# Performance work log

Measured on AMD Instinct MI355X. Metric: run time of the kernel, lower is better.

## Reference

```python
import jax, jax.numpy as jnp
import numpy as np

N = 100000   # nodes
E = 1600000  # edges (before self-loops)
H1, C1 = 8, 16   # conv1: heads=8, out_channels=16
H2, C2 = 1, 1    # conv2: heads=1, out_channels=1
NEG_SLOPE = 0.2
EPS = 1e-16


def setup_inputs() -> dict:
    key = jax.random.key(0)
    ks = jax.random.split(key, 10)
    s = 0.3
    return {
        "x": jax.random.normal(ks[0], (N, 1), jnp.float32),
        "edge_index": jax.random.randint(ks[1], (2, E), 0, N, dtype=jnp.int64),
        "W1": jax.random.normal(ks[2], (1, H1 * C1), jnp.float32) * s,
        "att_src1": jax.random.normal(ks[3], (1, H1, C1), jnp.float32) * s,
        "att_dst1": jax.random.normal(ks[4], (1, H1, C1), jnp.float32) * s,
        "b1": jax.random.normal(ks[5], (H1 * C1,), jnp.float32) * s,
        "W2": jax.random.normal(ks[6], (H1 * C1, H2 * C2), jnp.float32) * s,
        "att_src2": jax.random.normal(ks[7], (1, H2, C2), jnp.float32) * s,
        "att_dst2": jax.random.normal(ks[8], (1, H2, C2), jnp.float32) * s,
        "b2": jax.random.normal(ks[9], (C2,), jnp.float32) * s,
    }


def gat_conv(x, src, dst, W, att_src, att_dst, bias, heads, ch, concat):
    # Linear projection, split into heads: [N, H, C]
    h = (x @ W).reshape(-1, heads, ch)
    # Per-node attention logits: [N, H]
    a_src = (h * att_src).sum(-1)
    a_dst = (h * att_dst).sum(-1)
    # Edge-wise score with LeakyReLU: [E, H]
    e = jax.nn.leaky_relu(a_src[src] + a_dst[dst], NEG_SLOPE)
    # Segment softmax over incoming edges of each dst node
    m = jax.ops.segment_max(e, dst, num_segments=N)
    ex = jnp.exp(e - m[dst])
    denom = jax.ops.segment_sum(ex, dst, num_segments=N)
    alpha = ex / (denom[dst] + EPS)                      # [E, H]
    # Weighted scatter-add aggregation: [N, H, C]
    out = jax.ops.segment_sum(h[src] * alpha[:, :, None], dst, num_segments=N)
    out = out.reshape(-1, heads * ch) if concat else out.mean(axis=1)
    return out + bias


def reference(x, edge_index, W1, att_src1, att_dst1, b1, W2, att_src2, att_dst2, b2):
    # PyG GATConv default add_self_loops=True
    loop = jnp.arange(N, dtype=edge_index.dtype)
    src = jnp.concatenate([edge_index[0], loop])
    dst = jnp.concatenate([edge_index[1], loop])
    # dropout p=0.6 is identity in eval mode
    h = gat_conv(x, src, dst, W1, att_src1, att_dst1, b1, H1, C1, concat=True)
    h = jax.nn.elu(h)
    out = gat_conv(h, src, dst, W2, att_src2, att_dst2, b2, H2, C2, concat=False)
    return out  # [N, 1]
```

## Files before the change

kernel.cpp:

```cpp
#include <hip/hip_runtime.h>

#define NEG_SLOPE 0.2f
#define EPSV 1e-16f
#define NHEADS 8
#define NCH 16
#define BKT_SHIFT 7
#define BKT_NODES 128
#define CAP 4096
#define BIN_EPB 4096
#define MAX_BKT 800

__global__ __launch_bounds__(256) void gat_bin_kernel(
        const int* __restrict__ ei, int E, int nbuckets,
        int* __restrict__ bkt_cnt, unsigned int* __restrict__ binned) {
    __shared__ int hist[MAX_BKT];
    __shared__ int gbase[MAX_BKT];
    int t = threadIdx.x;
    for (int i = t; i < nbuckets; i += 256) hist[i] = 0;
    __syncthreads();
    int base = blockIdx.x * BIN_EPB;
    int lr[BIN_EPB / 256];
#pragma unroll
    for (int k = 0; k < BIN_EPB / 1024; ++k) {
        int idx = base + k * 1024 + t * 4;
        if (idx + 3 < E) {
            int4 d4 = *(const int4*)(ei + E + idx);
            lr[4 * k + 0] = atomicAdd(&hist[d4.x >> BKT_SHIFT], 1);
            lr[4 * k + 1] = atomicAdd(&hist[d4.y >> BKT_SHIFT], 1);
            lr[4 * k + 2] = atomicAdd(&hist[d4.z >> BKT_SHIFT], 1);
            lr[4 * k + 3] = atomicAdd(&hist[d4.w >> BKT_SHIFT], 1);
        } else {
            for (int u = 0; u < 4; ++u)
                if (idx + u < E)
                    lr[4 * k + u] = atomicAdd(&hist[ei[E + idx + u] >> BKT_SHIFT], 1);
        }
    }
    __syncthreads();
    for (int i = t; i < nbuckets; i += 256) {
        int c = hist[i];
        gbase[i] = c ? (i * CAP + atomicAdd(&bkt_cnt[i], c)) : 0;
    }
    __syncthreads();
#pragma unroll
    for (int k = 0; k < BIN_EPB / 1024; ++k) {
        int idx = base + k * 1024 + t * 4;
        if (idx + 3 < E) {
            int4 s4 = *(const int4*)(ei + idx);
            int4 d4 = *(const int4*)(ei + E + idx);
            binned[gbase[d4.x >> BKT_SHIFT] + lr[4 * k + 0]] =
                ((unsigned int)s4.x << BKT_SHIFT) | (unsigned int)(d4.x & (BKT_NODES - 1));
            binned[gbase[d4.y >> BKT_SHIFT] + lr[4 * k + 1]] =
                ((unsigned int)s4.y << BKT_SHIFT) | (unsigned int)(d4.y & (BKT_NODES - 1));
            binned[gbase[d4.z >> BKT_SHIFT] + lr[4 * k + 2]] =
                ((unsigned int)s4.z << BKT_SHIFT) | (unsigned int)(d4.z & (BKT_NODES - 1));
            binned[gbase[d4.w >> BKT_SHIFT] + lr[4 * k + 3]] =
                ((unsigned int)s4.w << BKT_SHIFT) | (unsigned int)(d4.w & (BKT_NODES - 1));
        } else {
            for (int u = 0; u < 4; ++u)
                if (idx + u < E) {
                    unsigned int s = (unsigned int)ei[idx + u];
                    int d = ei[E + idx + u];
                    binned[gbase[d >> BKT_SHIFT] + lr[4 * k + u]] =
                        (s << BKT_SHIFT) | (unsigned int)(d & (BKT_NODES - 1));
                }
        }
    }
}

__global__ __launch_bounds__(256) void gat_gather1_kernel(
        int N, const float* __restrict__ x,
        unsigned int* __restrict__ binned, const int* __restrict__ bkt_cnt,
        const float* __restrict__ W1, const float* __restrict__ as1,
        const float* __restrict__ ad1, const float* __restrict__ b1,
        const float* __restrict__ W2, float* __restrict__ h2out,
        int* __restrict__ row_start, int* __restrict__ row_deg) {
    __shared__ unsigned int ed[CAP];
    __shared__ int cnt[BKT_NODES], offs[BKT_NODES], cur[BKT_NODES];
    __shared__ float xloc[BKT_NODES];
    __shared__ float sS1[NHEADS], sD1[NHEADS];
    int b = blockIdx.x, t = threadIdx.x;
    if (t < NHEADS) {
        float s = 0.f, d = 0.f;
        for (int c = 0; c < NCH; ++c) {
            float w = W1[t * NCH + c];
            s += w * as1[t * NCH + c];
            d += w * ad1[t * NCH + c];
        }
        sS1[t] = s; sD1[t] = d;
    }
    if (t < BKT_NODES) {
        int node = (b << BKT_SHIFT) + t;
        xloc[t] = (node < N) ? x[node] : 0.f;
        cnt[t] = 0;
    }
    __syncthreads();
    int nE = bkt_cnt[b]; if (nE > CAP) nE = CAP;
    const unsigned int* bb = binned + (size_t)b * CAP;
    for (int j0 = 0; j0 < nE; j0 += 1024) {
        int idx = j0 + t * 4;
        if (idx + 3 < nE) {
            uint4 qv = *(const uint4*)(bb + idx);
            atomicAdd(&cnt[qv.x & (BKT_NODES - 1)], 1);
            atomicAdd(&cnt[qv.y & (BKT_NODES - 1)], 1);
            atomicAdd(&cnt[qv.z & (BKT_NODES - 1)], 1);
            atomicAdd(&cnt[qv.w & (BKT_NODES - 1)], 1);
        } else {
            for (int u = 0; u < 4; ++u)
                if (idx + u < nE) atomicAdd(&cnt[bb[idx + u] & (BKT_NODES - 1)], 1);
        }
    }
    __syncthreads();
    if (t < BKT_NODES) offs[t] = cnt[t];
    __syncthreads();
    for (int o = 1; o < BKT_NODES; o <<= 1) {
        int v = (t < BKT_NODES && t >= o) ? offs[t - o] : 0;
        __syncthreads();
        if (t < BKT_NODES) offs[t] += v;
        __syncthreads();
    }
    if (t < BKT_NODES) cur[t] = offs[t] - cnt[t];
    __syncthreads();
    for (int j0 = 0; j0 < nE; j0 += 1024) {
        int idx = j0 + t * 4;
        if (idx + 3 < nE) {
            uint4 qv = *(const uint4*)(bb + idx);
            ed[atomicAdd(&cur[qv.x & (BKT_NODES - 1)], 1)] = qv.x >> BKT_SHIFT;
            ed[atomicAdd(&cur[qv.y & (BKT_NODES - 1)], 1)] = qv.y >> BKT_SHIFT;
            ed[atomicAdd(&cur[qv.z & (BKT_NODES - 1)], 1)] = qv.z >> BKT_SHIFT;
            ed[atomicAdd(&cur[qv.w & (BKT_NODES - 1)], 1)] = qv.w >> BKT_SHIFT;
        } else {
            for (int u = 0; u < 4; ++u)
                if (idx + u < nE) {
                    unsigned int v = bb[idx + u];
                    ed[atomicAdd(&cur[v & (BKT_NODES - 1)], 1)] = v >> BKT_SHIFT;
                }
        }
    }
    __syncthreads();
    for (int j0 = 0; j0 < nE; j0 += 1024) {
        int idx = j0 + t * 4;
        if (idx + 3 < nE) {
            *(uint4*)(binned + (size_t)b * CAP + idx) = *(const uint4*)(ed + idx);
        } else {
            for (int u = 0; u < 4; ++u)
                if (idx + u < nE) binned[(size_t)b * CAP + idx + u] = ed[idx + u];
        }
    }
    int loc = t >> 1;
    int q = t & 1;
    int deg = cnt[loc];
    int ob = offs[loc] - deg;
    int lo = ob + ((deg * q) >> 1);
    int hi = ob + ((deg * (q + 1)) >> 1);
    float xd = xloc[loc];
    float S1[NHEADS], A[NHEADS], den[NHEADS], num[NHEADS];
#pragma unroll
    for (int h = 0; h < NHEADS; ++h) {
        S1[h] = sS1[h];
        A[h] = xd * sD1[h];
        den[h] = 0.f;
        num[h] = 0.f;
    }
    int j = lo;
    for (; j + 2 <= hi; j += 2) {
        unsigned int e0 = ed[j], e1 = ed[j + 1];
        float x0 = x[e0], x1 = x[e1];
#pragma unroll
        for (int h = 0; h < NHEADS; ++h) {
            float ea = x0 * S1[h] + A[h]; ea = ea > 0.f ? ea : NEG_SLOPE * ea;
            float eb = x1 * S1[h] + A[h]; eb = eb > 0.f ? eb : NEG_SLOPE * eb;
            float fa = __expf(ea), fb = __expf(eb);
            den[h] += fa + fb;
            num[h] += fa * x0 + fb * x1;
        }
    }
    if (j < hi) {
        unsigned int e0 = ed[j];
        float x0 = x[e0];
#pragma unroll
        for (int h = 0; h < NHEADS; ++h) {
            float ea = x0 * S1[h] + A[h];
            ea = ea > 0.f ? ea : NEG_SLOPE * ea;
            float fa = __expf(ea);
            den[h] += fa;
            num[h] += fa * x0;
        }
    }
#pragma unroll
    for (int h = 0; h < NHEADS; ++h) {
        den[h] += __shfl_xor(den[h], 1);
        num[h] += __shfl_xor(num[h], 1);
    }
    if (q == 0) {
        int node = (b << BKT_SHIFT) + loc;
        if (node < N) {
            row_start[node] = b * CAP + ob;
            row_deg[node] = deg;
            float xn = xd;
            float acc = 0.f;
#pragma unroll
            for (int h = 0; h < NHEADS; ++h) {
                float e = xn * (S1[h] + sD1[h]);
                e = e > 0.f ? e : NEG_SLOPE * e;
                float ex = __expf(e);
                float dsum = den[h] + ex + EPSV;
                float nsum = num[h] + ex * xn;
                float z = nsum / dsum;
#pragma unroll
                for (int c = 0; c < NCH; ++c) {
                    int k = h * NCH + c;
                    float vv = W1[k] * z + b1[k];
                    vv = vv > 0.f ? vv : (__expf(vv) - 1.f);
                    acc += vv * W2[k];
                }
            }
            h2out[node] = acc;
        }
    }
}

__global__ __launch_bounds__(256) void gat_gather2_kernel(
        int N, const float* __restrict__ h2,
        const unsigned int* __restrict__ binned,
        const int* __restrict__ row_start, const int* __restrict__ row_deg,
        const float* __restrict__ as2p, const float* __restrict__ ad2p,
        const float* __restrict__ b2, float* __restrict__ out) {
    int g = blockIdx.x * blockDim.x + threadIdx.x;
    int n = g >> 1;
    int q = g & 1;
    bool valid = (n < N);
    int nc = valid ? n : 0;
    float a_s = as2p[0], a_d = ad2p[0];
    float hn = h2[nc];
    float adc = hn * a_d;
    int st = row_start[nc];
    int dg = valid ? row_deg[nc] : 0;
    int lo = st + ((dg * q) >> 1);
    int hi = st + ((dg * (q + 1)) >> 1);
    float den = 0.f, num = 0.f;
    int j = lo;
    for (; j + 2 <= hi; j += 2) {
        unsigned int e0 = binned[j], e1 = binned[j + 1];
        float h0 = h2[e0], h1 = h2[e1];
        float ea = h0 * a_s + adc; ea = ea > 0.f ? ea : NEG_SLOPE * ea;
        float eb = h1 * a_s + adc; eb = eb > 0.f ? eb : NEG_SLOPE * eb;
        float fa = __expf(ea), fb = __expf(eb);
        den += fa + fb;
        num += fa * h0 + fb * h1;
    }
    if (j < hi) {
        unsigned int e0 = binned[j];
        float h0 = h2[e0];
        float ea = h0 * a_s + adc;
        ea = ea > 0.f ? ea : NEG_SLOPE * ea;
        float fa = __expf(ea);
        den += fa;
        num += fa * h0;
    }
    den += __shfl_xor(den, 1);
    num += __shfl_xor(num, 1);
    if (q == 0 && valid) {
        float e = hn * (a_s + a_d);
        e = e > 0.f ? e : NEG_SLOPE * e;
        float ex = __expf(e);
        out[n] = (num + ex * hn) / (den + ex + EPSV) + b2[0];
    }
}

extern "C" void kernel_launch(void* const* d_in, const int* in_sizes, int n_in,
                              void* d_out, int out_size, void* d_ws, size_t ws_size,
                              hipStream_t stream) {
    const float* x   = (const float*)d_in[0];
    const int*   ei  = (const int*)d_in[1];
    const float* W1  = (const float*)d_in[2];
    const float* as1 = (const float*)d_in[3];
    const float* ad1 = (const float*)d_in[4];
    const float* b1  = (const float*)d_in[5];
    const float* W2  = (const float*)d_in[6];
    const float* as2 = (const float*)d_in[7];
    const float* ad2 = (const float*)d_in[8];
    const float* b2  = (const float*)d_in[9];
    float* out = (float*)d_out;

    int N = in_sizes[0];
    int E = in_sizes[1] / 2;

    int nbuckets = (N + BKT_NODES - 1) >> BKT_SHIFT;
    int nbin     = (E + BIN_EPB - 1) / BIN_EPB;
    int nb2      = (2 * N + 255) / 256;

    float* h2        = (float*)d_ws;
    int*   row_start = (int*)(h2 + N);
    int*   row_deg   = row_start + N;
    int*   bkt_cnt   = row_deg + N;
    size_t ofs = ((size_t)3 * N + nbuckets + 3) & ~(size_t)3;
    unsigned int* binned = (unsigned int*)d_ws + ofs;

    hipMemsetAsync(bkt_cnt, 0, (size_t)nbuckets * sizeof(int), stream);

    gat_bin_kernel<<<nbin, 256, 0, stream>>>(ei, E, nbuckets, bkt_cnt, binned);
    gat_gather1_kernel<<<nbuckets, 256, 0, stream>>>(N, x, binned, bkt_cnt,
                                                     W1, as1, ad1, b1, W2,
                                                     h2, row_start, row_deg);
    gat_gather2_kernel<<<nb2, 256, 0, stream>>>(N, h2, binned, row_start, row_deg,
                                                as2, ad2, b2, out);
}
```

Before: 141.2 us.

## Shard bucket counters, drop CSR writeback, and make layer-2 gather bucket-local

The binning kernel now spreads its global atomic counters over four shards per bucket, each with its own 1024-entry sub-region, to reduce contention on the per-bucket counters. The first gather kernel no longer writes the sorted edge list back to global memory or emits row_start/row_deg, and it replaces the multi-barrier shared-memory scan with a wavefront shuffle scan. The second layer's gather now processes each bucket's unsorted edges directly with shared-memory float atomics into per-node accumulators. This trades the global writeback for LDS atomic contention, and caps each shard at 1024 edges, which could drop edges if a shard overflows.

```diff
diff --git a/kernel.cpp b/kernel.cpp
--- a/kernel.cpp
+++ b/kernel.cpp
@@ -7,6 +7,8 @@
 #define BKT_SHIFT 7
 #define BKT_NODES 128
 #define CAP 4096
+#define QCAP 1024
+#define NSHARD 4
 #define BIN_EPB 4096
 #define MAX_BKT 800
 
@@ -16,6 +18,7 @@
     __shared__ int hist[MAX_BKT];
     __shared__ int gbase[MAX_BKT];
     int t = threadIdx.x;
+    int s = blockIdx.x & (NSHARD - 1);
     for (int i = t; i < nbuckets; i += 256) hist[i] = 0;
     __syncthreads();
     int base = blockIdx.x * BIN_EPB;
@@ -38,7 +41,8 @@
     __syncthreads();
     for (int i = t; i < nbuckets; i += 256) {
         int c = hist[i];
-        gbase[i] = c ? (i * CAP + atomicAdd(&bkt_cnt[i], c)) : 0;
+        gbase[i] = c ? (i * CAP + s * QCAP + atomicAdd(&bkt_cnt[i * NSHARD + s], c))
+                     : 0;
     }
     __syncthreads();
 #pragma unroll
@@ -58,10 +62,10 @@
         } else {
             for (int u = 0; u < 4; ++u)
                 if (idx + u < E) {
-                    unsigned int s = (unsigned int)ei[idx + u];
+                    unsigned int sv = (unsigned int)ei[idx + u];
                     int d = ei[E + idx + u];
                     binned[gbase[d >> BKT_SHIFT] + lr[4 * k + u]] =
-                        (s << BKT_SHIFT) | (unsigned int)(d & (BKT_NODES - 1));
+                        (sv << BKT_SHIFT) | (unsigned int)(d & (BKT_NODES - 1));
                 }
         }
     }
@@ -69,15 +73,15 @@
 
 __global__ __launch_bounds__(256) void gat_gather1_kernel(
         int N, const float* __restrict__ x,
-        unsigned int* __restrict__ binned, const int* __restrict__ bkt_cnt,
+        const unsigned int* __restrict__ binned, const int* __restrict__ bkt_cnt,
         const float* __restrict__ W1, const float* __restrict__ as1,
         const float* __restrict__ ad1, const float* __restrict__ b1,
-        const float* __restrict__ W2, float* __restrict__ h2out,
-        int* __restrict__ row_start, int* __restrict__ row_deg) {
+        const float* __restrict__ W2, float* __restrict__ h2out) {
     __shared__ unsigned int ed[CAP];
     __shared__ int cnt[BKT_NODES], offs[BKT_NODES], cur[BKT_NODES];
     __shared__ float xloc[BKT_NODES];
     __shared__ float sS1[NHEADS], sD1[NHEADS];
+    __shared__ int wtot;
     int b = blockIdx.x, t = threadIdx.x;
     if (t < NHEADS) {
         float s = 0.f, d = 0.f;
@@ -94,62 +98,73 @@
         cnt[t] = 0;
     }
     __syncthreads();
-    int nE = bkt_cnt[b]; if (nE > CAP) nE = CAP;
-    const unsigned int* bb = binned + (size_t)b * CAP;
-    for (int j0 = 0; j0 < nE; j0 += 1024) {
-        int idx = j0 + t * 4;
-        if (idx + 3 < nE) {
-            uint4 qv = *(const uint4*)(bb + idx);
-            atomicAdd(&cnt[qv.x & (BKT_NODES - 1)], 1);
-            atomicAdd(&cnt[qv.y & (BKT_NODES - 1)], 1);
-            atomicAdd(&cnt[qv.z & (BKT_NODES - 1)], 1);
-            atomicAdd(&cnt[qv.w & (BKT_NODES - 1)], 1);
-        } else {
-            for (int u = 0; u < 4; ++u)
-                if (idx + u < nE) atomicAdd(&cnt[bb[idx + u] & (BKT_NODES - 1)], 1);
-        }
-    }
-    __syncthreads();
-    if (t < BKT_NODES) offs[t] = cnt[t];
-    __syncthreads();
-    for (int o = 1; o < BKT_NODES; o <<= 1) {
-        int v = (t < BKT_NODES && t >= o) ? offs[t - o] : 0;
+    int nq[NSHARD];
+#pragma unroll
+    for (int s = 0; s < NSHARD; ++s) {
+        int v = bkt_cnt[b * NSHARD + s];
+        nq[s] = v > QCAP ? QCAP : v;
+    }
+#pragma unroll
+    for (int s = 0; s < NSHARD; ++s) {
+        const unsigned int* bq = binned + (size_t)b * CAP + s * QCAP;
+        int nE = nq[s];
+        for (int idx = t * 4; idx < nE; idx += 1024) {
+            if (idx + 3 < nE) {
+                uint4 qv = *(const uint4*)(bq + idx);
+                atomicAdd(&cnt[qv.x & (BKT_NODES - 1)], 1);
+                atomicAdd(&cnt[qv.y & (BKT_NODES - 1)], 1);
+                atomicAdd(&cnt[qv.z & (BKT_NODES - 1)], 1);
+                atomicAdd(&cnt[qv.w & (BKT_NODES - 1)], 1);
+            } else {
+                for (int u = 0; u < 4; ++u)
+                    if (idx + u < nE) atomicAdd(&cnt[bq[idx + u] & (BKT_NODES - 1)], 1);
+            }
+        }
+    }
+    __syncthreads();
+    {
+        int c = (t < BKT_NODES) ? cnt[t] : 0;
+        int lane = t & 63;
+        int v = c;
+#pragma unroll
+        for (int o = 1; o < 64; o <<= 1) {
+            int u = __shfl_up(v, o);
+            if (lane >= o) v += u;
+        }
+        if (t == 63) wtot = v;
         __syncthreads();
-        if (t < BKT_NODES) offs[t] += v;
-        __syncthreads();
-    }
-    if (t < BKT_NODES) cur[t] = offs[t] - cnt[t];
-    __syncthreads();
-    for (int j0 = 0; j0 < nE; j0 += 1024) {
-        int idx = j0 + t * 4;
-        if (idx + 3 < nE) {
-            uint4 qv = *(const uint4*)(bb + idx);
-            ed[atomicAdd(&cur[qv.x & (BKT_NODES - 1)], 1)] = qv.x >> BKT_SHIFT;
-            ed[atomicAdd(&cur[qv.y & (BKT_NODES - 1)], 1)] = qv.y >> BKT_SHIFT;
-            ed[atomicAdd(&cur[qv.z & (BKT_NODES - 1)], 1)] = qv.z >> BKT_SHIFT;
-            ed[atomicAdd(&cur[qv.w & (BKT_NODES - 1)], 1)] = qv.w >> BKT_SHIFT;
-        } else {
-            for (int u = 0; u < 4; ++u)
-                if (idx + u < nE) {
-                    unsigned int v = bb[idx + u];
-                    ed[atomicAdd(&cur[v & (BKT_NODES - 1)], 1)] = v >> BKT_SHIFT;
-                }
-        }
-    }
-    __syncthreads();
-    for (int j0 = 0; j0 < nE; j0 += 1024) {
-        int idx = j0 + t * 4;
-        if (idx + 3 < nE) {
-            *(uint4*)(binned + (size_t)b * CAP + idx) = *(const uint4*)(ed + idx);
-        } else {
-            for (int u = 0; u < 4; ++u)
-                if (idx + u < nE) binned[(size_t)b * CAP + idx + u] = ed[idx + u];
-        }
-    }
+        if (t < BKT_NODES) {
+            int incl = v + ((t >= 64) ? wtot : 0);
+            offs[t] = incl - c;
+            cur[t] = incl - c;
+        }
+    }
+    __syncthreads();
+#pragma unroll
+    for (int s = 0; s < NSHARD; ++s) {
+        const unsigned int* bq = binned + (size_t)b * CAP + s * QCAP;
+        int nE = nq[s];
+        for (int idx = t * 4; idx < nE; idx += 1024) {
+            if (idx + 3 < nE) {
+                uint4 qv = *(const uint4*)(bq + idx);
+                ed[atomicAdd(&cur[qv.x & (BKT_NODES - 1)], 1)] = qv.x >> BKT_SHIFT;
+                ed[atomicAdd(&cur[qv.y & (BKT_NODES - 1)], 1)] = qv.y >> BKT_SHIFT;
+                ed[atomicAdd(&cur[qv.z & (BKT_NODES - 1)], 1)] = qv.z >> BKT_SHIFT;
+                ed[atomicAdd(&cur[qv.w & (BKT_NODES - 1)], 1)] = qv.w >> BKT_SHIFT;
+            } else {
+                for (int u = 0; u < 4; ++u)
+                    if (idx + u < nE) {
+                        unsigned int v = bq[idx + u];
+                        ed[atomicAdd(&cur[v & (BKT_NODES - 1)], 1)] = v >> BKT_SHIFT;
+                    }
+            }
+        }
+    }
+    __syncthreads();
     int loc = t >> 1;
     int q = t & 1;
     int deg = cnt[loc];
-    int ob = offs[loc] - deg;
+    int ob = offs[loc];
     int lo = ob + ((deg * q) >> 1);
     int hi = ob + ((deg * (q + 1)) >> 1);
     float xd = xloc[loc];
@@ -194,8 +209,6 @@
     if (q == 0) {
         int node = (b << BKT_SHIFT) + loc;
         if (node < N) {
-            row_start[node] = b * CAP + ob;
-            row_deg[node] = deg;
             float xn = xd;
             float acc = 0.f;
 #pragma unroll
@@ -221,49 +234,55 @@
 
 __global__ __launch_bounds__(256) void gat_gather2_kernel(
         int N, const float* __restrict__ h2,
-        const unsigned int* __restrict__ binned,
-        const int* __restrict__ row_start, const int* __restrict__ row_deg,
+        const unsigned int* __restrict__ binned, const int* __restrict__ bkt_cnt,
         const float* __restrict__ as2p, const float* __restrict__ ad2p,
         const float* __restrict__ b2, float* __restrict__ out) {
-    int g = blockIdx.x * blockDim.x + threadIdx.x;
-    int n = g >> 1;
-    int q = g & 1;
-    bool valid = (n < N);
-    int nc = valid ? n : 0;
+    __shared__ float den2[BKT_NODES], num2[BKT_NODES], hloc[BKT_NODES];
+    int b = blockIdx.x, t = threadIdx.x;
+    if (t < BKT_NODES) {
+        int node = (b << BKT_SHIFT) + t;
+        hloc[t] = (node < N) ? h2[node] : 0.f;
+        den2[t] = 0.f;
+        num2[t] = 0.f;
+    }
     float a_s = as2p[0], a_d = ad2p[0];
-    float hn = h2[nc];
-    float adc = hn * a_d;
-    int st = row_start[nc];
-    int dg = valid ? row_deg[nc] : 0;
-    int lo = st + ((dg * q) >> 1);
-    int hi = st + ((dg * (q + 1)) >> 1);
-    float den = 0.f, num = 0.f;
-    int j = lo;
-    for (; j + 2 <= hi; j += 2) {
-        unsigned int e0 = binned[j], e1 = binned[j + 1];
-        float h0 = h2[e0], h1 = h2[e1];
-        float ea = h0 * a_s + adc; ea = ea > 0.f ? ea : NEG_SLOPE * ea;
-        float eb = h1 * a_s + adc; eb = eb > 0.f ? eb : NEG_SLOPE * eb;
-        float fa = __expf(ea), fb = __expf(eb);
-        den += fa + fb;
-        num += fa * h0 + fb * h1;
-    }
-    if (j < hi) {
-        unsigned int e0 = binned[j];
-        float h0 = h2[e0];
-        float ea = h0 * a_s + adc;
-        ea = ea > 0.f ? ea : NEG_SLOPE * ea;
-        float fa = __expf(ea);
-        den += fa;
-        num += fa * h0;
-    }
-    den += __shfl_xor(den, 1);
-    num += __shfl_xor(num, 1);
-    if (q == 0 && valid) {
-        float e = hn * (a_s + a_d);
-        e = e > 0.f ? e : NEG_SLOPE * e;
-        float ex = __expf(e);
-        out[n] = (num + ex * hn) / (den + ex + EPSV) + b2[0];
+    __syncthreads();
+#pragma unroll
+    for (int s = 0; s < NSHARD; ++s) {
+        int nE = bkt_cnt[b * NSHARD + s];
+        if (nE > QCAP) nE = QCAP;
+        const unsigned int* bq = binned + (size_t)b * CAP + s * QCAP;
+        for (int idx = t * 4; idx < nE; idx += 1024) {
+            unsigned int v[4];
+            int nv = 0;
+            if (idx + 3 < nE) {
+                uint4 qv = *(const uint4*)(bq + idx);
+                v[0] = qv.x; v[1] = qv.y; v[2] = qv.z; v[3] = qv.w; nv = 4;
+            } else {
+                for (int u = 0; u < 4; ++u)
+                    if (idx + u < nE) v[nv++] = bq[idx + u];
+            }
+            for (int u = 0; u < nv; ++u) {
+                int loc = v[u] & (BKT_NODES - 1);
+                float hs = h2[v[u] >> BKT_SHIFT];
+                float e = hs * a_s + hloc[loc] * a_d;
+                e = e > 0.f ? e : NEG_SLOPE * e;
+                float ex = __expf(e);
+                atomicAdd(&den2[loc], ex);
+                atomicAdd(&num2[loc], ex * hs);
+            }
+        }
+    }
+    __syncthreads();
+    if (t < BKT_NODES) {
+        int node = (b << BKT_SHIFT) + t;
+        if (node < N) {
+            float hn = hloc[t];
+            float e = hn * (a_s + a_d);
+            e = e > 0.f ? e : NEG_SLOPE * e;
+            float ex = __expf(e);
+            out[node] = (num2[t] + ex * hn) / (den2[t] + ex + EPSV) + b2[0];
+        }
     }
 }
 
@@ -287,21 +306,17 @@
 
     int nbuckets = (N + BKT_NODES - 1) >> BKT_SHIFT;
     int nbin     = (E + BIN_EPB - 1) / BIN_EPB;
-    int nb2      = (2 * N + 255) / 256;
-
-    float* h2        = (float*)d_ws;
-    int*   row_start = (int*)(h2 + N);
-    int*   row_deg   = row_start + N;
-    int*   bkt_cnt   = row_deg + N;
-    size_t ofs = ((size_t)3 * N + nbuckets + 3) & ~(size_t)3;
+
+    float* h2      = (float*)d_ws;
+    int*   bkt_cnt = (int*)(h2 + N);
+    size_t ofs = ((size_t)N + (size_t)NSHARD * nbuckets + 3) & ~(size_t)3;
     unsigned int* binned = (unsigned int*)d_ws + ofs;
 
-    hipMemsetAsync(bkt_cnt, 0, (size_t)nbuckets * sizeof(int), stream);
+    hipMemsetAsync(bkt_cnt, 0, (size_t)NSHARD * nbuckets * sizeof(int), stream);
 
     gat_bin_kernel<<<nbin, 256, 0, stream>>>(ei, E, nbuckets, bkt_cnt, binned);
     gat_gather1_kernel<<<nbuckets, 256, 0, stream>>>(N, x, binned, bkt_cnt,
-                                                     W1, as1, ad1, b1, W2,
-                                                     h2, row_start, row_deg);
-    gat_gather2_kernel<<<nb2, 256, 0, stream>>>(N, h2, binned, row_start, row_deg,
-                                                as2, ad2, b2, out);
+                                                     W1, as1, ad1, b1, W2, h2);
+    gat_gather2_kernel<<<nbuckets, 256, 0, stream>>>(N, h2, binned, bkt_cnt,
+                                                     as2, ad2, b2, out);
 }
```

Result: slower. 153.8 us (+9.0%).

## Shard per-bucket global counters across eight sub-queues and use wave-shuffle scan

Applied to the files above, without the earlier changes.

The binning kernel now spreads each bucket's global atomic counter across eight shards chosen by block index, and each shard writes into its own 512-slot sub-region of the bucket. The aim is to cut contention on the global atomics when many blocks append to the same bucket. The gather kernel reads the eight shard counts and skips the unused gaps between sub-regions. It also replaces the shared-memory Hillis-Steele prefix scan with a wavefront shuffle scan to remove barriers. The cost is a per-shard capacity of 512 edges, which can overflow if the edge distribution is skewed, and some wasted reads over partially filled sub-regions.

```diff
diff --git a/kernel.cpp b/kernel.cpp
--- a/kernel.cpp
+++ b/kernel.cpp
@@ -6,6 +6,9 @@
 #define NCH 16
 #define BKT_SHIFT 7
 #define BKT_NODES 128
+#define NSHARD 8
+#define QSHIFT 9
+#define QCAP 512
 #define CAP 4096
 #define BIN_EPB 4096
 #define MAX_BKT 800
@@ -16,6 +19,7 @@
     __shared__ int hist[MAX_BKT];
     __shared__ int gbase[MAX_BKT];
     int t = threadIdx.x;
+    int s = blockIdx.x & (NSHARD - 1);
     for (int i = t; i < nbuckets; i += 256) hist[i] = 0;
     __syncthreads();
     int base = blockIdx.x * BIN_EPB;
@@ -38,7 +42,8 @@
     __syncthreads();
     for (int i = t; i < nbuckets; i += 256) {
         int c = hist[i];
-        gbase[i] = c ? (i * CAP + atomicAdd(&bkt_cnt[i], c)) : 0;
+        gbase[i] = c ? (i * CAP + s * QCAP + atomicAdd(&bkt_cnt[i * NSHARD + s], c))
+                     : 0;
     }
     __syncthreads();
 #pragma unroll
@@ -58,10 +63,10 @@
         } else {
             for (int u = 0; u < 4; ++u)
                 if (idx + u < E) {
-                    unsigned int s = (unsigned int)ei[idx + u];
+                    unsigned int sv = (unsigned int)ei[idx + u];
                     int d = ei[E + idx + u];
                     binned[gbase[d >> BKT_SHIFT] + lr[4 * k + u]] =
-                        (s << BKT_SHIFT) | (unsigned int)(d & (BKT_NODES - 1));
+                        (sv << BKT_SHIFT) | (unsigned int)(d & (BKT_NODES - 1));
                 }
         }
     }
@@ -78,6 +83,8 @@
     __shared__ int cnt[BKT_NODES], offs[BKT_NODES], cur[BKT_NODES];
     __shared__ float xloc[BKT_NODES];
     __shared__ float sS1[NHEADS], sD1[NHEADS];
+    __shared__ int snq[NSHARD];
+    __shared__ int wtot;
     int b = blockIdx.x, t = threadIdx.x;
     if (t < NHEADS) {
         float s = 0.f, d = 0.f;
@@ -88,68 +95,82 @@
         }
         sS1[t] = s; sD1[t] = d;
     }
+    if (t < NSHARD) {
+        int v = bkt_cnt[b * NSHARD + t];
+        snq[t] = v > QCAP ? QCAP : v;
+    }
     if (t < BKT_NODES) {
         int node = (b << BKT_SHIFT) + t;
         xloc[t] = (node < N) ? x[node] : 0.f;
         cnt[t] = 0;
     }
     __syncthreads();
-    int nE = bkt_cnt[b]; if (nE > CAP) nE = CAP;
     const unsigned int* bb = binned + (size_t)b * CAP;
-    for (int j0 = 0; j0 < nE; j0 += 1024) {
-        int idx = j0 + t * 4;
-        if (idx + 3 < nE) {
-            uint4 qv = *(const uint4*)(bb + idx);
+    for (int vb = t * 4; vb < CAP; vb += 1024) {
+        int nE = snq[vb >> QSHIFT];
+        int w = vb & (QCAP - 1);
+        if (w + 3 < nE) {
+            uint4 qv = *(const uint4*)(bb + vb);
             atomicAdd(&cnt[qv.x & (BKT_NODES - 1)], 1);
             atomicAdd(&cnt[qv.y & (BKT_NODES - 1)], 1);
             atomicAdd(&cnt[qv.z & (BKT_NODES - 1)], 1);
             atomicAdd(&cnt[qv.w & (BKT_NODES - 1)], 1);
         } else {
             for (int u = 0; u < 4; ++u)
-                if (idx + u < nE) atomicAdd(&cnt[bb[idx + u] & (BKT_NODES - 1)], 1);
-        }
-    }
-    __syncthreads();
-    if (t < BKT_NODES) offs[t] = cnt[t];
-    __syncthreads();
-    for (int o = 1; o < BKT_NODES; o <<= 1) {
-        int v = (t < BKT_NODES && t >= o) ? offs[t - o] : 0;
+                if (w + u < nE) atomicAdd(&cnt[bb[vb + u] & (BKT_NODES - 1)], 1);
+        }
+    }
+    __syncthreads();
+    {
+        int c = (t < BKT_NODES) ? cnt[t] : 0;
+        int lane = t & 63;
+        int v = c;
+#pragma unroll
+        for (int o = 1; o < 64; o <<= 1) {
+            int u = __shfl_up(v, o);
+            if (lane >= o) v += u;
+        }
+        if (t == 63) wtot = v;
         __syncthreads();
-        if (t < BKT_NODES) offs[t] += v;
-        __syncthreads();
-    }
-    if (t < BKT_NODES) cur[t] = offs[t] - cnt[t];
-    __syncthreads();
-    for (int j0 = 0; j0 < nE; j0 += 1024) {
-        int idx = j0 + t * 4;
-        if (idx + 3 < nE) {
-            uint4 qv = *(const uint4*)(bb + idx);
+        if (t < BKT_NODES) {
+            int incl = v + ((t >= 64) ? wtot : 0);
+            offs[t] = incl - c;
+            cur[t] = incl - c;
+        }
+    }
+    __syncthreads();
+    for (int vb = t * 4; vb < CAP; vb += 1024) {
+        int nE = snq[vb >> QSHIFT];
+        int w = vb & (QCAP - 1);
+        if (w + 3 < nE) {
+            uint4 qv = *(const uint4*)(bb + vb);
             ed[atomicAdd(&cur[qv.x & (BKT_NODES - 1)], 1)] = qv.x >> BKT_SHIFT;
             ed[atomicAdd(&cur[qv.y & (BKT_NODES - 1)], 1)] = qv.y >> BKT_SHIFT;
             ed[atomicAdd(&cur[qv.z & (BKT_NODES - 1)], 1)] = qv.z >> BKT_SHIFT;
             ed[atomicAdd(&cur[qv.w & (BKT_NODES - 1)], 1)] = qv.w >> BKT_SHIFT;
         } else {
             for (int u = 0; u < 4; ++u)
-                if (idx + u < nE) {
-                    unsigned int v = bb[idx + u];
+                if (w + u < nE) {
+                    unsigned int v = bb[vb + u];
                     ed[atomicAdd(&cur[v & (BKT_NODES - 1)], 1)] = v >> BKT_SHIFT;
                 }
         }
     }
     __syncthreads();
-    for (int j0 = 0; j0 < nE; j0 += 1024) {
-        int idx = j0 + t * 4;
-        if (idx + 3 < nE) {
+    int nT = snq[0] + snq[1] + snq[2] + snq[3] +
+             snq[4] + snq[5] + snq[6] + snq[7];
+    for (int idx = t * 4; idx < nT; idx += 1024) {
+        if (idx + 3 < nT) {
             *(uint4*)(binned + (size_t)b * CAP + idx) = *(const uint4*)(ed + idx);
         } else {
             for (int u = 0; u < 4; ++u)
-                if (idx + u < nE) binned[(size_t)b * CAP + idx + u] = ed[idx + u];
+                if (idx + u < nT) binned[(size_t)b * CAP + idx + u] = ed[idx + u];
         }
     }
     int loc = t >> 1;
     int q = t & 1;
     int deg = cnt[loc];
-    int ob = offs[loc] - deg;
+    int ob = offs[loc];
     int lo = ob + ((deg * q) >> 1);
     int hi = ob + ((deg * (q + 1)) >> 1);
     float xd = xloc[loc];
@@ -293,10 +314,10 @@
     int*   row_start = (int*)(h2 + N);
     int*   row_deg   = row_start + N;
     int*   bkt_cnt   = row_deg + N;
-    size_t ofs = ((size_t)3 * N + nbuckets + 3) & ~(size_t)3;
+    size_t ofs = ((size_t)3 * N + (size_t)NSHARD * nbuckets + 3) & ~(size_t)3;
     unsigned int* binned = (unsigned int*)d_ws + ofs;
 
-    hipMemsetAsync(bkt_cnt, 0, (size_t)nbuckets * sizeof(int), stream);
+    hipMemsetAsync(bkt_cnt, 0, (size_t)NSHARD * nbuckets * sizeof(int), stream);
 
     gat_bin_kernel<<<nbin, 256, 0, stream>>>(ei, E, nbuckets, bkt_cnt, binned);
     gat_gather1_kernel<<<nbuckets, 256, 0, stream>>>(N, x, binned, bkt_cnt,
```

Measured after the change: 142.5 us. No clear change (+0.9%).
